# Kernel optimization log

Hardware: AMD Instinct MI355X
Metric: run time of the kernel (lower is better)

The kernel has to match this reference:

```python
import jax, jax.numpy as jnp
import numpy as np

N_NODES = 50000
N_EDGES = 640000
HIDDEN = 128
EDGE_EMB_DIM = 8
NUM_EDGE_TYPES = 16


def setup_inputs() -> dict:
    key = jax.random.key(0)
    ks = jax.random.split(key, 10)
    x = jax.random.normal(ks[0], (N_NODES, HIDDEN), dtype=jnp.float32)
    edge_index = jax.random.randint(ks[1], (2, N_EDGES), 0, N_NODES, dtype=jnp.int64)
    edge_attr = jax.random.randint(ks[2], (N_EDGES, 3), 0, NUM_EDGE_TYPES, dtype=jnp.int64)
    # learned params
    emb = jax.random.normal(ks[3], (NUM_EDGE_TYPES, EDGE_EMB_DIM), dtype=jnp.float32) * 0.1
    We = jax.random.normal(ks[4], (EDGE_EMB_DIM, HIDDEN), dtype=jnp.float32) * (1.0 / np.sqrt(EDGE_EMB_DIM))
    be = jnp.zeros((HIDDEN,), dtype=jnp.float32)
    W1 = jax.random.normal(ks[5], (HIDDEN, HIDDEN), dtype=jnp.float32) * (1.0 / np.sqrt(HIDDEN))
    b1 = jnp.zeros((HIDDEN,), dtype=jnp.float32)
    W2 = jax.random.normal(ks[6], (HIDDEN, HIDDEN), dtype=jnp.float32) * (1.0 / np.sqrt(HIDDEN))
    b2 = jnp.zeros((HIDDEN,), dtype=jnp.float32)
    eps = jnp.zeros((), dtype=jnp.float32)  # train_eps=True, init 0
    return {"x": x, "edge_index": edge_index, "edge_attr": edge_attr,
            "emb": emb, "We": We, "be": be,
            "W1": W1, "b1": b1, "W2": W2, "b2": b2, "eps": eps}


def reference(x, edge_index, edge_attr, emb, We, be, W1, b1, W2, b2, eps):
    n_nodes = x.shape[0]
    # edge-type hash -> embedding lookup [E, edge_emb_dim]
    h = (edge_attr[:, 0] + 3 * edge_attr[:, 1] + 7 * edge_attr[:, 2]) % NUM_EDGE_TYPES
    e = emb[h]
    # GINEConv internal lin: edge_dim -> hidden
    e_proj = e @ We + be  # [E, H]
    src, dst = edge_index[0], edge_index[1]  # j -> i
    # message: relu(x_j + lin(e)); aggregate: scatter-sum at target node i
    msg = jax.nn.relu(x[src] + e_proj)  # [E, H]
    aggr = jax.ops.segment_sum(msg, dst, num_segments=n_nodes)  # [N, H]
    # update: mlp((1 + eps) * x_i + aggr)
    z = (1.0 + eps) * x + aggr
    out = jax.nn.relu(z @ W1 + b1) @ W2 + b2
    return out
```

## Files before the change

### kernel.cpp

```cpp
#include <hip/hip_runtime.h>

#define H       128
#define NNODES  50000
#define NEDGES  640000
#define NTYPES  16
#define EDIM    8
#define BCAP    64

#define BKT_BLOCKS  2500
#define XB_BLOCKS   3125
#define PROJ_BLOCKS 8
#define PACK_BLOCKS 16
#define PREP_BLOCKS (BKT_BLOCKS + XB_BLOCKS + PROJ_BLOCKS + PACK_BLOCKS)

typedef __attribute__((ext_vector_type(8))) __bf16 bf16x8;
typedef __attribute__((ext_vector_type(4))) float  f32x4;

__device__ __forceinline__ unsigned short f2bf(float f) {
    unsigned int u = __float_as_uint(f);
    u += 0x7fffu + ((u >> 16) & 1u);
    return (unsigned short)(u >> 16);
}

__global__ __launch_bounds__(256) void prep_kernel(
        const float* __restrict__ x, unsigned short* __restrict__ xb,
        const int* __restrict__ edge_index, const int* __restrict__ edge_attr,
        int* __restrict__ cursor, unsigned int* __restrict__ packed,
        const float* __restrict__ emb, const float* __restrict__ We,
        const float* __restrict__ be, float* __restrict__ proj,
        const float* __restrict__ W1, const float* __restrict__ W2,
        unsigned short* __restrict__ w1p, unsigned short* __restrict__ w2p) {
    const int b = blockIdx.x;
    const int t = threadIdx.x;

    if (b < BKT_BLOCKS) {
        int e = b * 256 + t;
        int src = edge_index[e];
        int dst = edge_index[NEDGES + e];
        int a0 = edge_attr[e * 3 + 0];
        int a1 = edge_attr[e * 3 + 1];
        int a2 = edge_attr[e * 3 + 2];
        unsigned int h = (unsigned int)(a0 + 3 * a1 + 7 * a2) & (NTYPES - 1);
        int pos = atomicAdd(&cursor[dst], 1);
        if (pos < BCAP)
            packed[((unsigned)dst << 6) + pos] = (unsigned int)src | (h << 16);
    } else if (b < BKT_BLOCKS + XB_BLOCKS) {
        int i = ((b - BKT_BLOCKS) * 256 + t) * 8;
        float4 a = *(const float4*)(x + i);
        float4 c = *(const float4*)(x + i + 4);
        int4 o;
        o.x = (int)((unsigned int)f2bf(a.x) | ((unsigned int)f2bf(a.y) << 16));
        o.y = (int)((unsigned int)f2bf(a.z) | ((unsigned int)f2bf(a.w) << 16));
        o.z = (int)((unsigned int)f2bf(c.x) | ((unsigned int)f2bf(c.y) << 16));
        o.w = (int)((unsigned int)f2bf(c.z) | ((unsigned int)f2bf(c.w) << 16));
        *(int4*)(xb + i) = o;
    } else if (b < BKT_BLOCKS + XB_BLOCKS + PROJ_BLOCKS) {
        int id = (b - BKT_BLOCKS - XB_BLOCKS) * 256 + t;
        int ty = id >> 7;
        int f  = id & (H - 1);
        float acc = be[f];
#pragma unroll
        for (int d = 0; d < EDIM; ++d)
            acc += emb[ty * EDIM + d] * We[d * H + f];
        proj[id] = acc;
    } else {
        int id = (b - BKT_BLOCKS - XB_BLOCKS - PROJ_BLOCKS) * 256 + t;
        const float* W = (id < 2048) ? W1 : W2;
        unsigned short* P = (id < 2048) ? w1p : w2p;
        int q = id & 2047;
        int lane = q & 63;
        int kc = (q >> 6) & 3;
        int c  = q >> 8;
        int n = c * 16 + (lane & 15);
        int kbase = kc * 32 + (lane >> 4) * 8;
#pragma unroll
        for (int j = 0; j < 8; ++j)
            P[q * 8 + j] = f2bf(W[(kbase + j) * H + n]);
    }
}

__global__ __launch_bounds__(256) void gine_fused_kernel(
        const unsigned short* __restrict__ xb,
        const int* __restrict__ deg,
        const unsigned int* __restrict__ packed,
        const float* __restrict__ proj,
        const float* __restrict__ epsp,
        const unsigned short* __restrict__ w1p,
        const unsigned short* __restrict__ w2p,
        const float* __restrict__ b1,
        const float* __restrict__ b2,
        float* __restrict__ out) {
    __shared__ float projL[NTYPES * H];
    __shared__ unsigned short Tz[16 * 136];
    __shared__ unsigned short Th[16 * 136];
    const int t = threadIdx.x;
    ((float4*)projL)[t]       = ((const float4*)proj)[t];
    ((float4*)projL)[t + 256] = ((const float4*)proj)[t + 256];
    __syncthreads();

    const int w = t >> 6, lane = t & 63;
    const int lane2 = lane * 2;
    const int nodeBase = blockIdx.x * 16;
    const float scale = 1.0f + *epsp;

#pragma unroll
    for (int i = 0; i < 4; ++i) {
        const int row = w * 4 + i;
        const int node = nodeBase + row;
        const int s = node << 6;
        int d = deg[node]; if (d > BCAP) d = BCAP;
        const int e = s + d;
        float ax = 0.f, ay = 0.f;
        int j = s;
        const int n4 = s + (d & ~3);
        for (; j < n4; j += 4) {
            unsigned int p0 = packed[j + 0];
            unsigned int p1 = packed[j + 1];
            unsigned int p2 = packed[j + 2];
            unsigned int p3 = packed[j + 3];
            unsigned int g0 = *(const unsigned int*)(xb + ((p0 & 0xffffu) << 7) + lane2);
            unsigned int g1 = *(const unsigned int*)(xb + ((p1 & 0xffffu) << 7) + lane2);
            unsigned int g2 = *(const unsigned int*)(xb + ((p2 & 0xffffu) << 7) + lane2);
            unsigned int g3 = *(const unsigned int*)(xb + ((p3 & 0xffffu) << 7) + lane2);
            float2 q0 = *(const float2*)(projL + ((p0 >> 16) << 7) + lane2);
            float2 q1 = *(const float2*)(projL + ((p1 >> 16) << 7) + lane2);
            float2 q2 = *(const float2*)(projL + ((p2 >> 16) << 7) + lane2);
            float2 q3 = *(const float2*)(projL + ((p3 >> 16) << 7) + lane2);
            ax += fmaxf(__uint_as_float(g0 << 16) + q0.x, 0.f)
                + fmaxf(__uint_as_float(g1 << 16) + q1.x, 0.f)
                + fmaxf(__uint_as_float(g2 << 16) + q2.x, 0.f)
                + fmaxf(__uint_as_float(g3 << 16) + q3.x, 0.f);
            ay += fmaxf(__uint_as_float(g0 & 0xffff0000u) + q0.y, 0.f)
                + fmaxf(__uint_as_float(g1 & 0xffff0000u) + q1.y, 0.f)
                + fmaxf(__uint_as_float(g2 & 0xffff0000u) + q2.y, 0.f)
                + fmaxf(__uint_as_float(g3 & 0xffff0000u) + q3.y, 0.f);
        }
        for (; j < e; ++j) {
            unsigned int p0 = packed[j];
            unsigned int g0 = *(const unsigned int*)(xb + ((p0 & 0xffffu) << 7) + lane2);
            float2 q0 = *(const float2*)(projL + ((p0 >> 16) << 7) + lane2);
            ax += fmaxf(__uint_as_float(g0 << 16) + q0.x, 0.f);
            ay += fmaxf(__uint_as_float(g0 & 0xffff0000u) + q0.y, 0.f);
        }
        unsigned int go = *(const unsigned int*)(xb + ((unsigned)node << 7) + lane2);
        float zx = scale * __uint_as_float(go << 16) + ax;
        float zy = scale * __uint_as_float(go & 0xffff0000u) + ay;
        *(unsigned int*)(Tz + row * 136 + lane2) =
            (unsigned int)f2bf(zx) | ((unsigned int)f2bf(zy) << 16);
    }
    __syncthreads();

    const int m = lane & 15, quad = lane >> 4;

    bf16x8 a[4];
#pragma unroll
    for (int kc = 0; kc < 4; ++kc)
        a[kc] = *(const bf16x8*)(Tz + m * 136 + kc * 32 + quad * 8);

    const bf16x8* w1f = (const bf16x8*)w1p;
#pragma unroll
    for (int cc = 0; cc < 2; ++cc) {
        const int c = w + cc * 4;
        f32x4 acc = {0.f, 0.f, 0.f, 0.f};
#pragma unroll
        for (int kc = 0; kc < 4; ++kc)
            acc = __builtin_amdgcn_mfma_f32_16x16x32_bf16(
                      a[kc], w1f[(c * 4 + kc) * 64 + lane], acc, 0, 0, 0);
        const int col = c * 16 + m;
        const float bias = b1[col];
#pragma unroll
        for (int r = 0; r < 4; ++r)
            Th[(quad * 4 + r) * 136 + col] = f2bf(fmaxf(acc[r] + bias, 0.0f));
    }
    __syncthreads();

    bf16x8 ha[4];
#pragma unroll
    for (int kc = 0; kc < 4; ++kc)
        ha[kc] = *(const bf16x8*)(Th + m * 136 + kc * 32 + quad * 8);

    const bf16x8* w2f = (const bf16x8*)w2p;
#pragma unroll
    for (int cc = 0; cc < 2; ++cc) {
        const int c = w + cc * 4;
        f32x4 acc = {0.f, 0.f, 0.f, 0.f};
#pragma unroll
        for (int kc = 0; kc < 4; ++kc)
            acc = __builtin_amdgcn_mfma_f32_16x16x32_bf16(
                      ha[kc], w2f[(c * 4 + kc) * 64 + lane], acc, 0, 0, 0);
        const int col = c * 16 + m;
        const float bias = b2[col];
#pragma unroll
        for (int r = 0; r < 4; ++r)
            out[(size_t)(nodeBase + quad * 4 + r) * H + col] = acc[r] + bias;
    }
}

extern "C" void kernel_launch(void* const* d_in, const int* in_sizes, int n_in,
                              void* d_out, int out_size, void* d_ws, size_t ws_size,
                              hipStream_t stream) {
    const float* x          = (const float*)d_in[0];
    const int*   edge_index = (const int*)  d_in[1];
    const int*   edge_attr  = (const int*)  d_in[2];
    const float* emb        = (const float*)d_in[3];
    const float* We         = (const float*)d_in[4];
    const float* be         = (const float*)d_in[5];
    const float* W1         = (const float*)d_in[6];
    const float* b1         = (const float*)d_in[7];
    const float* W2         = (const float*)d_in[8];
    const float* b2         = (const float*)d_in[9];
    const float* eps        = (const float*)d_in[10];
    float* out = (float*)d_out;

    char* ws = (char*)d_ws;
    size_t off = 0;
    float* proj    = (float*)(ws + off); off += (size_t)NTYPES * H * 4;
    int*   cursor  = (int*)  (ws + off); off += (size_t)NNODES * 4;
    unsigned int*   packed = (unsigned int*)(ws + off);   off += (size_t)NNODES * BCAP * 4;
    unsigned short* xb     = (unsigned short*)(ws + off); off += (size_t)NNODES * H * 2;
    unsigned short* w1p    = (unsigned short*)(ws + off); off += 2048 * 8 * 2;
    unsigned short* w2p    = (unsigned short*)(ws + off); off += 2048 * 8 * 2;

    hipMemsetAsync(cursor, 0, (size_t)NNODES * sizeof(int), stream);

    prep_kernel<<<PREP_BLOCKS, 256, 0, stream>>>(
        x, xb, edge_index, edge_attr, cursor, packed,
        emb, We, be, proj, W1, W2, w1p, w2p);

    gine_fused_kernel<<<NNODES / 16, 256, 0, stream>>>(
        xb, cursor, packed, proj, eps, w1p, w2p, b1, b2, out);
}
```

Before: 176.8 us.

## Process four nodes per wave concurrently with 16-byte gathers per lane

The aggregation phase is remapped so each wavefront handles four nodes at once, 16 lanes per node, each lane gathering 8 bf16 features with a 16-byte load. Before, a wave walked its four nodes one after another with 4-byte loads per lane. The projection table in shared memory is padded to a 132-float row stride to reduce bank conflicts on the wider reads. This gives more memory-level parallelism and fewer, wider gather instructions. In exchange, lanes within a wave now diverge on different node degrees, and there is less unrolling per node.

```diff
diff --git a/kernel.cpp b/kernel.cpp
--- a/kernel.cpp
+++ b/kernel.cpp
@@ -6,6 +6,7 @@
 #define NTYPES  16
 #define EDIM    8
 #define BCAP    64
+#define PSTRIDE 132
 
 #define BKT_BLOCKS  2500
 #define XB_BLOCKS   3125
@@ -20,6 +21,18 @@
     unsigned int u = __float_as_uint(f);
     u += 0x7fffu + ((u >> 16) & 1u);
     return (unsigned short)(u >> 16);
+}
+
+__device__ __forceinline__ void acc8(uint4 g, float4 qa, float4 qb,
+                                     float4& A, float4& B) {
+    A.x += fmaxf(__uint_as_float(g.x << 16)         + qa.x, 0.f);
+    A.y += fmaxf(__uint_as_float(g.x & 0xffff0000u) + qa.y, 0.f);
+    A.z += fmaxf(__uint_as_float(g.y << 16)         + qa.z, 0.f);
+    A.w += fmaxf(__uint_as_float(g.y & 0xffff0000u) + qa.w, 0.f);
+    B.x += fmaxf(__uint_as_float(g.z << 16)         + qb.x, 0.f);
+    B.y += fmaxf(__uint_as_float(g.z & 0xffff0000u) + qb.y, 0.f);
+    B.z += fmaxf(__uint_as_float(g.w << 16)         + qb.z, 0.f);
+    B.w += fmaxf(__uint_as_float(g.w & 0xffff0000u) + qb.w, 0.f);
 }
 
 __global__ __launch_bounds__(256) void prep_kernel(
@@ -90,63 +103,67 @@
         const float* __restrict__ b1,
         const float* __restrict__ b2,
         float* __restrict__ out) {
-    __shared__ float projL[NTYPES * H];
+    __shared__ float projL[NTYPES * PSTRIDE];
     __shared__ unsigned short Tz[16 * 136];
     __shared__ unsigned short Th[16 * 136];
     const int t = threadIdx.x;
-    ((float4*)projL)[t]       = ((const float4*)proj)[t];
-    ((float4*)projL)[t + 256] = ((const float4*)proj)[t + 256];
+#pragma unroll
+    for (int i = 0; i < 2; ++i) {
+        int idx = t + i * 256;
+        int r = idx >> 5, c4 = idx & 31;
+        *(float4*)(projL + r * PSTRIDE + c4 * 4) = ((const float4*)proj)[idx];
+    }
     __syncthreads();
 
     const int w = t >> 6, lane = t & 63;
-    const int lane2 = lane * 2;
+    const int grp = lane >> 4, sub = lane & 15;
     const int nodeBase = blockIdx.x * 16;
     const float scale = 1.0f + *epsp;
 
-#pragma unroll
-    for (int i = 0; i < 4; ++i) {
-        const int row = w * 4 + i;
-        const int node = nodeBase + row;
-        const int s = node << 6;
-        int d = deg[node]; if (d > BCAP) d = BCAP;
-        const int e = s + d;
-        float ax = 0.f, ay = 0.f;
-        int j = s;
-        const int n4 = s + (d & ~3);
-        for (; j < n4; j += 4) {
-            unsigned int p0 = packed[j + 0];
-            unsigned int p1 = packed[j + 1];
-            unsigned int p2 = packed[j + 2];
-            unsigned int p3 = packed[j + 3];
-            unsigned int g0 = *(const unsigned int*)(xb + ((p0 & 0xffffu) << 7) + lane2);
-            unsigned int g1 = *(const unsigned int*)(xb + ((p1 & 0xffffu) << 7) + lane2);
-            unsigned int g2 = *(const unsigned int*)(xb + ((p2 & 0xffffu) << 7) + lane2);
-            unsigned int g3 = *(const unsigned int*)(xb + ((p3 & 0xffffu) << 7) + lane2);
-            float2 q0 = *(const float2*)(projL + ((p0 >> 16) << 7) + lane2);
-            float2 q1 = *(const float2*)(projL + ((p1 >> 16) << 7) + lane2);
-            float2 q2 = *(const float2*)(projL + ((p2 >> 16) << 7) + lane2);
-            float2 q3 = *(const float2*)(projL + ((p3 >> 16) << 7) + lane2);
-            ax += fmaxf(__uint_as_float(g0 << 16) + q0.x, 0.f)
-                + fmaxf(__uint_as_float(g1 << 16) + q1.x, 0.f)
-                + fmaxf(__uint_as_float(g2 << 16) + q2.x, 0.f)
-                + fmaxf(__uint_as_float(g3 << 16) + q3.x, 0.f);
-            ay += fmaxf(__uint_as_float(g0 & 0xffff0000u) + q0.y, 0.f)
-                + fmaxf(__uint_as_float(g1 & 0xffff0000u) + q1.y, 0.f)
-                + fmaxf(__uint_as_float(g2 & 0xffff0000u) + q2.y, 0.f)
-                + fmaxf(__uint_as_float(g3 & 0xffff0000u) + q3.y, 0.f);
-        }
-        for (; j < e; ++j) {
-            unsigned int p0 = packed[j];
-            unsigned int g0 = *(const unsigned int*)(xb + ((p0 & 0xffffu) << 7) + lane2);
-            float2 q0 = *(const float2*)(projL + ((p0 >> 16) << 7) + lane2);
-            ax += fmaxf(__uint_as_float(g0 << 16) + q0.x, 0.f);
-            ay += fmaxf(__uint_as_float(g0 & 0xffff0000u) + q0.y, 0.f);
-        }
-        unsigned int go = *(const unsigned int*)(xb + ((unsigned)node << 7) + lane2);
-        float zx = scale * __uint_as_float(go << 16) + ax;
-        float zy = scale * __uint_as_float(go & 0xffff0000u) + ay;
-        *(unsigned int*)(Tz + row * 136 + lane2) =
-            (unsigned int)f2bf(zx) | ((unsigned int)f2bf(zy) << 16);
+    const int row  = w * 4 + grp;
+    const int node = nodeBase + row;
+    const int s = node << 6;
+    int d = deg[node]; if (d > BCAP) d = BCAP;
+    const int e = s + d;
+    const int sub8 = sub * 8;
+
+    float4 A = {0.f, 0.f, 0.f, 0.f}, B = {0.f, 0.f, 0.f, 0.f};
+    int j = s;
+    for (; j + 1 < e; j += 2) {
+        unsigned int p0 = packed[j];
+        unsigned int p1 = packed[j + 1];
+        uint4 g0 = *(const uint4*)(xb + ((p0 & 0xffffu) << 7) + sub8);
+        uint4 g1 = *(const uint4*)(xb + ((p1 & 0xffffu) << 7) + sub8);
+        const float* q0 = projL + (p0 >> 16) * PSTRIDE + sub8;
+        const float* q1 = projL + (p1 >> 16) * PSTRIDE + sub8;
+        float4 qa0 = *(const float4*)q0, qb0 = *(const float4*)(q0 + 4);
+        float4 qa1 = *(const float4*)q1, qb1 = *(const float4*)(q1 + 4);
+        acc8(g0, qa0, qb0, A, B);
+        acc8(g1, qa1, qb1, A, B);
+    }
+    if (j < e) {
+        unsigned int p0 = packed[j];
+        uint4 g0 = *(const uint4*)(xb + ((p0 & 0xffffu) << 7) + sub8);
+        const float* q0 = projL + (p0 >> 16) * PSTRIDE + sub8;
+        acc8(g0, *(const float4*)q0, *(const float4*)(q0 + 4), A, B);
+    }
+
+    {
+        uint4 go = *(const uint4*)(xb + ((unsigned)node << 7) + sub8);
+        float z0 = scale * __uint_as_float(go.x << 16)         + A.x;
+        float z1 = scale * __uint_as_float(go.x & 0xffff0000u) + A.y;
+        float z2 = scale * __uint_as_float(go.y << 16)         + A.z;
+        float z3 = scale * __uint_as_float(go.y & 0xffff0000u) + A.w;
+        float z4 = scale * __uint_as_float(go.z << 16)         + B.x;
+        float z5 = scale * __uint_as_float(go.z & 0xffff0000u) + B.y;
+        float z6 = scale * __uint_as_float(go.w << 16)         + B.z;
+        float z7 = scale * __uint_as_float(go.w & 0xffff0000u) + B.w;
+        uint4 o;
+        o.x = (unsigned int)f2bf(z0) | ((unsigned int)f2bf(z1) << 16);
+        o.y = (unsigned int)f2bf(z2) | ((unsigned int)f2bf(z3) << 16);
+        o.z = (unsigned int)f2bf(z4) | ((unsigned int)f2bf(z5) << 16);
+        o.w = (unsigned int)f2bf(z6) | ((unsigned int)f2bf(z7) << 16);
+        *(uint4*)(Tz + row * 136 + sub8) = o;
     }
     __syncthreads();
 
```

Result: no change. 177.4 us (+0.3%).
